# Performance work log

Hardware: AMD Instinct MI355X
Metric: run time of the kernel (lower is better)

The kernel has to match this reference:

```python
import jax, jax.numpy as jnp
import numpy as np

TOP_K = 2  # cfg.num_experts_per_tok
INIT_STD = 0.02


def setup_inputs() -> dict:
    key = jax.random.key(0)
    ks = jax.random.split(key, 6)
    B, S, D, F, E = 4, 2048, 1024, 4096, 8
    return {
        "residual": jax.random.normal(ks[0], (B, S, D), dtype=jnp.float32),
        "W_router": jax.random.normal(ks[1], (E, D), dtype=jnp.float32) * INIT_STD,
        "W_in": jax.random.normal(ks[2], (E, D, F), dtype=jnp.float32) * INIT_STD,
        "b_in": jnp.zeros((E, F), dtype=jnp.float32),
        "W_out": jax.random.normal(ks[3], (E, F, D), dtype=jnp.float32) * INIT_STD,
        "b_out": jnp.zeros((E, D), dtype=jnp.float32),
    }


def reference(residual, W_router, W_in, b_in, W_out, b_out):
    B, S, D = residual.shape
    E = W_router.shape[0]
    x = residual.reshape(-1, D)                      # [T, D], T = B*S

    # Router: softmax over experts, pick top-k, renormalize selected weights.
    logits = jnp.einsum('td,ed->te', x, W_router)    # [T, E]
    probs = jax.nn.softmax(logits, axis=-1)
    top_w, top_i = jax.lax.top_k(probs, TOP_K)       # [T, K]
    top_w = top_w / jnp.sum(top_w, axis=-1, keepdims=True)

    # Dense combine weights [T, E]; zero for non-selected experts.
    combine = jnp.sum(jax.nn.one_hot(top_i, E, dtype=x.dtype) * top_w[..., None], axis=1)

    # Weighted sum of expert MLP outputs (GELU experts, exact erf as in torch).
    y = jnp.zeros_like(x)
    for e in range(E):  # small fixed expert count
        h = jax.nn.gelu(x @ W_in[e] + b_in[e], approximate=False)   # [T, F]
        y = y + combine[:, e:e + 1] * (h @ W_out[e] + b_out[e])     # [T, D]
    return y.reshape(B, S, D)
```

## Files before the change

kernel.cpp:

```cpp
#include <hip/hip_runtime.h>
#include <hip/hip_bf16.h>
#include <math.h>

#define T_TOK 8192
#define DMODEL 1024
#define FFN 4096
#define NEXP 8
#define NSLOT (T_TOK * 2)
#define MAXT 136

typedef _Float16 f16;
typedef _Float16 half8 __attribute__((ext_vector_type(8)));
typedef _Float16 half4 __attribute__((ext_vector_type(4)));
typedef float f32x4 __attribute__((ext_vector_type(4)));
typedef unsigned int u32;

__device__ __forceinline__ void gll16(const void* g, void* l) {
  __builtin_amdgcn_global_load_lds(
      (const __attribute__((address_space(1))) u32*)g,
      (__attribute__((address_space(3))) u32*)l, 16, 0, 0);
}

__device__ __forceinline__ float gelu_fast(float v) {
  float x = fabsf(v) * 0.70710678118654752f;
  float t = 1.0f / (1.0f + 0.3275911f * x);
  float poly = ((((1.061405429f * t - 1.453152027f) * t + 1.421413741f) * t -
                 0.284496736f) * t + 0.254829592f) * t;
  float erf_ = 1.0f - poly * __expf(-x * x);
  erf_ = copysignf(erf_, v);
  return 0.5f * v * (1.0f + erf_);
}

__device__ __forceinline__ float gelu_exact(float v) {
  return 0.5f * v * (1.0f + erff(v * 0.70710678118654752f));
}

__device__ __forceinline__ bool decode_tile(const int* __restrict__ counts,
                                            int tm, int& e, int& row0,
                                            int& nrows) {
  int acc = 0, off = 0;
#pragma unroll
  for (int i = 0; i < NEXP; i++) {
    int c = counts[i];
    int nt = (c + 127) >> 7;
    if (tm < acc + nt) {
      int lt = tm - acc;
      e = i; row0 = off + lt * 128; nrows = min(128, c - lt * 128);
      return true;
    }
    acc += nt; off += c;
  }
  return false;
}

__device__ __forceinline__ void transq_tile(const float* __restrict__ ip,
                                            f16* __restrict__ op, int R, int C,
                                            int r0, int c0, char* smemraw) {
  float* tile = (float*)smemraw;
  int tid = threadIdx.x;
  int q = tid & 15;
  int rr = tid >> 4;
#pragma unroll
  for (int p = 0; p < 8; p++) {
    int row = rr + p * 16;
    f32x4 v = *(const f32x4*)(ip + (size_t)(r0 + row) * C + c0 + q * 4);
    int qs = (q + (row >> 3)) & 15;
    *(f32x4*)(tile + row * 64 + qs * 4) = v;
  }
  __syncthreads();
#pragma unroll
  for (int p = 0; p < 4; p++) {
    int idx = tid + p * 256;
    int c = idx >> 4;
    int b = idx & 15;
    half8 h;
#pragma unroll
    for (int i = 0; i < 8; i++) {
      int row = b * 8 + i;
      int qs = (((c >> 2) + b) & 15);
      h[i] = (f16)tile[row * 64 + qs * 4 + (c & 3)];
    }
    __builtin_nontemporal_store(h, (half8*)(op + (size_t)(c0 + c) * R + r0 + b * 8));
  }
}

__global__ __launch_bounds__(256) void prepA_k(
    const float* __restrict__ x, const float* __restrict__ Wr,
    const float* __restrict__ Wi,
    int* __restrict__ sel_e, float* __restrict__ sel_w,
    f16* __restrict__ xh, f16* __restrict__ WiT) {
  __shared__ __align__(16) char smem[32768];
  if (blockIdx.x < 4096) {
    int e = blockIdx.x >> 9;
    int idx = blockIdx.x & 511;
    int rt = idx >> 6, ct = idx & 63;
    transq_tile(Wi + (size_t)e * DMODEL * FFN, WiT + (size_t)e * DMODEL * FFN,
                DMODEL, FFN, rt * 128, ct * 64, smem);
  } else {
    int rb = blockIdx.x - 4096;
    int t = rb * 4 + (threadIdx.x >> 6);
    int lane = threadIdx.x & 63;
    const float* xp = x + (size_t)t * DMODEL;
    f16* xhp = xh + (size_t)t * DMODEL;
    float p[NEXP];
#pragma unroll
    for (int e = 0; e < NEXP; e++) p[e] = 0.f;
#pragma unroll
    for (int q = 0; q < 4; q++) {
      f32x4 xv = *(const f32x4*)(xp + q * 256 + lane * 4);
      half4 h;
      h[0] = (f16)xv[0]; h[1] = (f16)xv[1]; h[2] = (f16)xv[2]; h[3] = (f16)xv[3];
      *(half4*)(xhp + q * 256 + lane * 4) = h;
#pragma unroll
      for (int e = 0; e < NEXP; e++) {
        const f32x4 wv = *(const f32x4*)(Wr + e * DMODEL + q * 256 + lane * 4);
        p[e] += xv[0] * wv[0] + xv[1] * wv[1] + xv[2] * wv[2] + xv[3] * wv[3];
      }
    }
#pragma unroll
    for (int off = 32; off; off >>= 1) {
#pragma unroll
      for (int e = 0; e < NEXP; e++) p[e] += __shfl_xor(p[e], off);
    }
    if (lane == 0) {
      float l0 = -1e30f, l1 = -1e30f;
      int e0 = 0, e1 = 1;
#pragma unroll
      for (int e = 0; e < NEXP; e++) {
        if (p[e] > l0) { l1 = l0; e1 = e0; l0 = p[e]; e0 = e; }
        else if (p[e] > l1) { l1 = p[e]; e1 = e; }
      }
      float r = expf(l1 - l0);
      float inv = 1.f / (1.f + r);
      sel_e[t * 2] = e0;     sel_w[t * 2] = inv;
      sel_e[t * 2 + 1] = e1; sel_w[t * 2 + 1] = r * inv;
    }
  }
}

__global__ __launch_bounds__(256) void count64_k(const int* __restrict__ sel_e,
                                                 int* __restrict__ counts) {
  __shared__ int lc[NEXP];
  int tid = threadIdx.x;
  if (tid < NEXP) lc[tid] = 0;
  __syncthreads();
  int v = sel_e[blockIdx.x * 256 + tid];
  atomicAdd(&lc[v], 1);
  __syncthreads();
  if (tid < NEXP) atomicAdd(&counts[tid], lc[tid]);
}

__global__ __launch_bounds__(256) void scatter_k(
    const int* __restrict__ sel_e, const float* __restrict__ sel_w,
    const int* __restrict__ counts, int* fill,
    int* __restrict__ row_tok, float* __restrict__ row_w,
    int* __restrict__ inv) {
  int s = blockIdx.x * 256 + threadIdx.x;
  int e = sel_e[s];
  int offs = 0;
#pragma unroll
  for (int i = 0; i < NEXP; i++) offs += (i < e) ? counts[i] : 0;
  int pos = atomicAdd(&fill[e], 1);
  int r = offs + pos;
  row_tok[r] = s >> 1;
  row_w[r] = sel_w[s];
  inv[s] = r;
}

__global__ __launch_bounds__(256, 3) void gemm1_k(
    const f16* __restrict__ Xh, const f16* __restrict__ Wt,
    const float* __restrict__ b_in, f16* __restrict__ H,
    const int* __restrict__ meta,
    const float* __restrict__ Wo, f16* __restrict__ WoT) {
  __shared__ __align__(16) char smem[36864];

  if (blockIdx.x >= MAXT * 32) {
    int bid = blockIdx.x - MAXT * 32;
    int e = bid >> 9;
    int idx = bid & 511;
    int rt = idx >> 4, ct = idx & 15;
    transq_tile(Wo + (size_t)e * DMODEL * FFN, WoT + (size_t)e * DMODEL * FFN,
                FFN, DMODEL, rt * 128, ct * 64, smem);
    return;
  }
  int bid2 = blockIdx.x;
  int xcd = bid2 & 7, bidx = bid2 >> 3;
  int wg = xcd * ((MAXT * 32) >> 3) + bidx;
  int tm = wg >> 5;
  int n0 = (wg & 31) * 128;
  int e, row0, nrows;
  if (!decode_tile(meta, tm, e, row0, nrows)) return;
  const int* row_tok = meta + 1024 + 2 * NSLOT;

  int tid = threadIdx.x, lane = tid & 63, wid = tid >> 6;
  int wrow = wid >> 1, wcol = wid & 1;
  int l15 = lane & 15, l4 = lane >> 4;

  u32 aoffs[4], boffs[4];
#pragma unroll
  for (int p = 0; p < 4; p++) {
    int L = tid + p * 256;
    int row = L >> 3, ch = L & 7;
    int cs = ch ^ (row & 7);
    aoffs[p] = (u32)(row_tok[min(row0 + row, NSLOT - 1)] * (DMODEL * 2) + cs * 16);
    boffs[p] = (u32)((e * FFN + n0 + row) * (DMODEL * 2) + cs * 16);
  }
  const char* gA = (const char*)Xh;
  const char* gB = (const char*)Wt;

  f32x4 acc[4][4];
#pragma unroll
  for (int m = 0; m < 4; m++)
#pragma unroll
    for (int n = 0; n < 4; n++) acc[m][n] = (f32x4)0.f;

  const int NT = DMODEL / 64;
  for (int kt = 0; kt < NT; ++kt) {
#pragma unroll
    for (int p = 0; p < 4; p++) {
      gll16(gA + aoffs[p], smem + (tid + p * 256) * 16);
      gll16(gB + boffs[p], smem + 16384 + (tid + p * 256) * 16);
      aoffs[p] += 128; boffs[p] += 128;
    }
    __syncthreads();
#pragma unroll
    for (int s = 0; s < 2; s++) {
      int swz = ((s * 4 + l4) ^ (l15 & 7)) << 4;
      const char* pA = smem + (wrow * 64 + l15) * 128 + swz;
      const char* pB = smem + 16384 + (wcol * 64 + l15) * 128 + swz;
      half8 a[4], b[4];
#pragma unroll
      for (int i = 0; i < 4; i++) a[i] = *(const half8*)(pA + i * 2048);
#pragma unroll
      for (int j = 0; j < 4; j++) b[j] = *(const half8*)(pB + j * 2048);
#pragma unroll
      for (int i = 0; i < 4; i++)
#pragma unroll
        for (int j = 0; j < 4; j++)
          acc[i][j] = __builtin_amdgcn_mfma_f32_16x16x32_f16(a[i], b[j], acc[i][j], 0, 0, 0);
    }
    __syncthreads();
  }

  char* wsm = smem + wid * 9216;
  float bias[4];
#pragma unroll
  for (int n = 0; n < 4; n++) bias[n] = b_in[e * FFN + n0 + wcol * 64 + n * 16 + l15];
#pragma unroll
  for (int m = 0; m < 4; m++)
#pragma unroll
    for (int n = 0; n < 4; n++)
#pragma unroll
      for (int j = 0; j < 4; j++) {
        int lrow = m * 16 + l4 * 4 + j;
        *(f16*)(wsm + lrow * 144 + (n * 16 + l15) * 2) =
            (f16)gelu_fast(acc[m][n][j] + bias[n]);
      }
#pragma unroll
  for (int p = 0; p < 8; ++p) {
    int lr = (lane >> 3) + p * 8;
    if (wrow * 64 + lr < nrows) {
      f32x4 v = *(const f32x4*)(wsm + lr * 144 + (lane & 7) * 16);
      __builtin_nontemporal_store(
          v, (f32x4*)(H + (size_t)(row0 + wrow * 64 + lr) * FFN + n0 +
                      wcol * 64 + (lane & 7) * 8));
    }
  }
}

__global__ __launch_bounds__(256, 3) void gemm2_k(
    const f16* __restrict__ H, const f16* __restrict__ Wt,
    const float* __restrict__ b_out, f16* __restrict__ Y0,
    f16* __restrict__ Y1, const int* __restrict__ meta) {
  int xcd = blockIdx.x & 7, bidx = blockIdx.x >> 3;
  int wg = xcd * (gridDim.x >> 3) + bidx;
  int tm = wg >> 4;
  int r4 = wg & 15;
  int n0 = (r4 & 7) * 128;
  int ks = r4 >> 3;
  int e, row0, nrows;
  if (!decode_tile(meta, tm, e, row0, nrows)) return;

  __shared__ __align__(16) char smem[36864];

  int tid = threadIdx.x, lane = tid & 63, wid = tid >> 6;
  int wrow = wid >> 1, wcol = wid & 1;
  int l15 = lane & 15, l4 = lane >> 4;
  u32 k0b = (u32)(ks * (FFN / 2) * 2);

  u32 aoffs[4], boffs[4];
#pragma unroll
  for (int p = 0; p < 4; p++) {
    int L = tid + p * 256;
    int row = L >> 3, ch = L & 7;
    int cs = ch ^ (row & 7);
    aoffs[p] = (u32)((u32)min(row0 + row, NSLOT - 1) * (FFN * 2) + k0b + cs * 16);
    boffs[p] = (u32)((u32)(e * DMODEL + n0 + row) * (FFN * 2) + k0b + cs * 16);
  }
  const char* gA = (const char*)H;
  const char* gB = (const char*)Wt;

  f32x4 acc[4][4];
#pragma unroll
  for (int m = 0; m < 4; m++)
#pragma unroll
    for (int n = 0; n < 4; n++) acc[m][n] = (f32x4)0.f;

  const int NT = (FFN / 2) / 64;
  for (int kt = 0; kt < NT; ++kt) {
#pragma unroll
    for (int p = 0; p < 4; p++) {
      gll16(gA + aoffs[p], smem + (tid + p * 256) * 16);
      gll16(gB + boffs[p], smem + 16384 + (tid + p * 256) * 16);
      aoffs[p] += 128; boffs[p] += 128;
    }
    __syncthreads();
#pragma unroll
    for (int s = 0; s < 2; s++) {
      int swz = ((s * 4 + l4) ^ (l15 & 7)) << 4;
      const char* pA = smem + (wrow * 64 + l15) * 128 + swz;
      const char* pB = smem + 16384 + (wcol * 64 + l15) * 128 + swz;
      half8 a[4], b[4];
#pragma unroll
      for (int i = 0; i < 4; i++) a[i] = *(const half8*)(pA + i * 2048);
#pragma unroll
      for (int j = 0; j < 4; j++) b[j] = *(const half8*)(pB + j * 2048);
#pragma unroll
      for (int i = 0; i < 4; i++)
#pragma unroll
        for (int j = 0; j < 4; j++)
          acc[i][j] = __builtin_amdgcn_mfma_f32_16x16x32_f16(a[i], b[j], acc[i][j], 0, 0, 0);
    }
    __syncthreads();
  }

  f16* Y = ks ? Y1 : Y0;
  char* wsm = smem + wid * 9216;
  float bias[4];
#pragma unroll
  for (int n = 0; n < 4; n++)
    bias[n] = (ks == 0) ? b_out[e * DMODEL + n0 + wcol * 64 + n * 16 + l15] : 0.f;
#pragma unroll
  for (int m = 0; m < 4; m++)
#pragma unroll
    for (int n = 0; n < 4; n++)
#pragma unroll
      for (int j = 0; j < 4; j++) {
        int lrow = m * 16 + l4 * 4 + j;
        *(f16*)(wsm + lrow * 144 + (n * 16 + l15) * 2) =
            (f16)(acc[m][n][j] + bias[n]);
      }
#pragma unroll
  for (int p = 0; p < 8; ++p) {
    int lr = (lane >> 3) + p * 8;
    if (wrow * 64 + lr < nrows) {
      f32x4 v = *(const f32x4*)(wsm + lr * 144 + (lane & 7) * 16);
      __builtin_nontemporal_store(
          v, (f32x4*)(Y + (size_t)(row0 + wrow * 64 + lr) * DMODEL + n0 +
                      wcol * 64 + (lane & 7) * 8));
    }
  }
}

__global__ __launch_bounds__(256) void combine_k(
    const f16* __restrict__ Y0, const f16* __restrict__ Y1,
    const int* __restrict__ inv, const float* __restrict__ row_w,
    float* __restrict__ out) {
  int t = blockIdx.x * 4 + (threadIdx.x >> 6);
  int lane = threadIdx.x & 63;
  int r0 = inv[2 * t], r1 = inv[2 * t + 1];
  float w0 = row_w[r0], w1 = row_w[r1];
  int d0 = lane * 16;
  const half8* a0 = (const half8*)(Y0 + (size_t)r0 * DMODEL + d0);
  const half8* a1 = (const half8*)(Y1 + (size_t)r0 * DMODEL + d0);
  const half8* b0 = (const half8*)(Y0 + (size_t)r1 * DMODEL + d0);
  const half8* b1 = (const half8*)(Y1 + (size_t)r1 * DMODEL + d0);
  float* op = out + (size_t)t * DMODEL + d0;
#pragma unroll
  for (int q = 0; q < 2; q++) {
    half8 x0 = a0[q], x1 = a1[q], y0 = b0[q], y1 = b1[q];
    float r[8];
#pragma unroll
    for (int i = 0; i < 8; i++)
      r[i] = w0 * ((float)x0[i] + (float)x1[i]) +
             w1 * ((float)y0[i] + (float)y1[i]);
    f32x4 v1 = {r[0], r[1], r[2], r[3]};
    f32x4 v2 = {r[4], r[5], r[6], r[7]};
    *(f32x4*)(op + q * 8) = v1;
    *(f32x4*)(op + q * 8 + 4) = v2;
  }
}

__global__ __launch_bounds__(256) void naive_k(
    const float* __restrict__ x, const float* __restrict__ W_in,
    const float* __restrict__ b_in, const float* __restrict__ W_out,
    const float* __restrict__ b_out, const int* __restrict__ sel_e,
    const float* __restrict__ sel_w, float* __restrict__ out) {
  int s = blockIdx.x;
  int t = s >> 1;
  int e = sel_e[s];
  float w = sel_w[s];
  __shared__ float xs[DMODEL];
  __shared__ float hs[FFN];
  int tid = threadIdx.x;
  for (int d = tid; d < DMODEL; d += 256) xs[d] = x[(size_t)t * DMODEL + d];
  __syncthreads();
  for (int f = tid; f < FFN; f += 256) {
    float a = b_in[e * FFN + f];
    const float* wp = W_in + (size_t)e * DMODEL * FFN + f;
    for (int d = 0; d < DMODEL; d++) a += xs[d] * wp[(size_t)d * FFN];
    hs[f] = gelu_exact(a);
  }
  __syncthreads();
  for (int d = tid; d < DMODEL; d += 256) {
    float a = b_out[e * DMODEL + d];
    const float* wp = W_out + (size_t)e * FFN * DMODEL + d;
    for (int f = 0; f < FFN; f++) a += hs[f] * wp[(size_t)f * DMODEL];
    atomicAdd(&out[(size_t)t * DMODEL + d], w * a);
  }
}

__global__ __launch_bounds__(256) void router_k(
    const float* __restrict__ x, const float* __restrict__ Wr,
    int* __restrict__ sel_e, float* __restrict__ sel_w) {
  int t = blockIdx.x * 4 + (threadIdx.x >> 6);
  int lane = threadIdx.x & 63;
  const float* xp = x + (size_t)t * DMODEL;
  float p[NEXP];
#pragma unroll
  for (int e = 0; e < NEXP; e++) p[e] = 0.f;
#pragma unroll
  for (int i = 0; i < DMODEL / 64; i++) {
    float xv = xp[lane + i * 64];
#pragma unroll
    for (int e = 0; e < NEXP; e++) p[e] += xv * Wr[e * DMODEL + lane + i * 64];
  }
#pragma unroll
  for (int off = 32; off; off >>= 1) {
#pragma unroll
    for (int e = 0; e < NEXP; e++) p[e] += __shfl_xor(p[e], off);
  }
  if (lane == 0) {
    float l0 = -1e30f, l1 = -1e30f;
    int e0 = 0, e1 = 1;
#pragma unroll
    for (int e = 0; e < NEXP; e++) {
      if (p[e] > l0) { l1 = l0; e1 = e0; l0 = p[e]; e0 = e; }
      else if (p[e] > l1) { l1 = p[e]; e1 = e; }
    }
    float r = expf(l1 - l0);
    float inv = 1.f / (1.f + r);
    sel_e[t * 2] = e0;     sel_w[t * 2] = inv;
    sel_e[t * 2 + 1] = e1; sel_w[t * 2 + 1] = r * inv;
  }
}

extern "C" void kernel_launch(void* const* d_in, const int* in_sizes, int n_in,
                              void* d_out, int out_size, void* d_ws, size_t ws_size,
                              hipStream_t stream) {
  const float* residual = (const float*)d_in[0];
  const float* W_router = (const float*)d_in[1];
  const float* W_in = (const float*)d_in[2];
  const float* b_in = (const float*)d_in[3];
  const float* W_out = (const float*)d_in[4];
  const float* b_out = (const float*)d_in[5];
  float* out = (float*)d_out;

  char* ws = (char*)d_ws;
  int* meta = (int*)ws;
  size_t off = (size_t)1 << 20;
  f16* Xh = (f16*)(ws + off); off += (size_t)T_TOK * DMODEL * 2;
  f16* Wih = (f16*)(ws + off); off += (size_t)NEXP * DMODEL * FFN * 2;
  f16* Woh = (f16*)(ws + off); off += (size_t)NEXP * DMODEL * FFN * 2;
  f16* H = (f16*)(ws + off); off += (size_t)NSLOT * FFN * 2;
  off += 65536;
  bool fast = ws_size >= off;

  f16* Y0 = Wih;
  f16* Y1 = Wih + (size_t)NSLOT * DMODEL;

  int* sel_e = meta + 1024;
  float* sel_w = (float*)(meta + 1024 + NSLOT);
  int* row_tok = meta + 1024 + 2 * NSLOT;
  float* row_w = (float*)(meta + 1024 + 3 * NSLOT);
  int* inv = meta + 1024 + 4 * NSLOT;

  if (fast) {
    hipMemsetAsync(meta, 0, 512, stream);
    prepA_k<<<4096 + T_TOK / 4, 256, 0, stream>>>(
        residual, W_router, W_in, sel_e, sel_w, Xh, Wih);
    count64_k<<<NSLOT / 256, 256, 0, stream>>>(sel_e, meta);
    scatter_k<<<NSLOT / 256, 256, 0, stream>>>(sel_e, sel_w, meta, meta + 64,
                                               row_tok, row_w, inv);
    gemm1_k<<<MAXT * 32 + 4096, 256, 0, stream>>>(Xh, Wih, b_in, H, meta,
                                                  W_out, Woh);
    gemm2_k<<<MAXT * 16, 256, 0, stream>>>(H, Woh, b_out, Y0, Y1, meta);
    combine_k<<<T_TOK / 4, 256, 0, stream>>>(Y0, Y1, inv, row_w, out);
  } else {
    hipMemsetAsync(d_out, 0, (size_t)out_size * sizeof(float), stream);
    router_k<<<T_TOK / 4, 256, 0, stream>>>(residual, W_router, sel_e, sel_w);
    naive_k<<<NSLOT, 256, 0, stream>>>(residual, W_in, b_in, W_out, b_out,
                                       sel_e, sel_w, out);
  }
}
```

Baseline: 512.6 us.

## Widen gemm1 tile to 128x256 with 512-thread blocks

Changes gemm1 from 256-thread blocks computing 128x128 tiles to 512-thread blocks (8 waves in a 2x4 grid) computing 128x256 tiles. Each A (token) tile is now reused across twice as many output columns, which halves the gathered A loads and the block count. The fused W_out transpose path gets a 512-thread variant, and the transposes now use plain stores instead of nontemporal ones. The 72KB shared memory request and launch_bounds(512,4) could limit occupancy or cause register spills.

```diff
diff --git a/kernel.cpp b/kernel.cpp
--- a/kernel.cpp
+++ b/kernel.cpp
@@ -53,16 +53,15 @@
   return false;
 }
 
-__device__ __forceinline__ void transq_tile(const float* __restrict__ ip,
-                                            f16* __restrict__ op, int R, int C,
-                                            int r0, int c0, char* smemraw) {
+__device__ __forceinline__ void transq_tile256(const float* __restrict__ ip,
+                                               f16* __restrict__ op, int R, int C,
+                                               int r0, int c0, char* smemraw) {
   float* tile = (float*)smemraw;
   int tid = threadIdx.x;
-  int q = tid & 15;
-  int rr = tid >> 4;
 #pragma unroll
   for (int p = 0; p < 8; p++) {
-    int row = rr + p * 16;
+    int idx = tid + p * 256;
+    int row = idx >> 4, q = idx & 15;
     f32x4 v = *(const f32x4*)(ip + (size_t)(r0 + row) * C + c0 + q * 4);
     int qs = (q + (row >> 3)) & 15;
     *(f32x4*)(tile + row * 64 + qs * 4) = v;
@@ -71,8 +70,7 @@
 #pragma unroll
   for (int p = 0; p < 4; p++) {
     int idx = tid + p * 256;
-    int c = idx >> 4;
-    int b = idx & 15;
+    int c = idx >> 4, b = idx & 15;
     half8 h;
 #pragma unroll
     for (int i = 0; i < 8; i++) {
@@ -80,7 +78,36 @@
       int qs = (((c >> 2) + b) & 15);
       h[i] = (f16)tile[row * 64 + qs * 4 + (c & 3)];
     }
-    __builtin_nontemporal_store(h, (half8*)(op + (size_t)(c0 + c) * R + r0 + b * 8));
+    *(half8*)(op + (size_t)(c0 + c) * R + r0 + b * 8) = h;
+  }
+}
+
+__device__ __forceinline__ void transq_tile512(const float* __restrict__ ip,
+                                               f16* __restrict__ op, int R, int C,
+                                               int r0, int c0, char* smemraw) {
+  float* tile = (float*)smemraw;
+  int tid = threadIdx.x;
+#pragma unroll
+  for (int p = 0; p < 4; p++) {
+    int idx = tid + p * 512;
+    int row = idx >> 4, q = idx & 15;
+    f32x4 v = *(const f32x4*)(ip + (size_t)(r0 + row) * C + c0 + q * 4);
+    int qs = (q + (row >> 3)) & 15;
+    *(f32x4*)(tile + row * 64 + qs * 4) = v;
+  }
+  __syncthreads();
+#pragma unroll
+  for (int p = 0; p < 2; p++) {
+    int idx = tid + p * 512;
+    int c = idx >> 4, b = idx & 15;
+    half8 h;
+#pragma unroll
+    for (int i = 0; i < 8; i++) {
+      int row = b * 8 + i;
+      int qs = (((c >> 2) + b) & 15);
+      h[i] = (f16)tile[row * 64 + qs * 4 + (c & 3)];
+    }
+    *(half8*)(op + (size_t)(c0 + c) * R + r0 + b * 8) = h;
   }
 }
 
@@ -94,8 +121,8 @@
     int e = blockIdx.x >> 9;
     int idx = blockIdx.x & 511;
     int rt = idx >> 6, ct = idx & 63;
-    transq_tile(Wi + (size_t)e * DMODEL * FFN, WiT + (size_t)e * DMODEL * FFN,
-                DMODEL, FFN, rt * 128, ct * 64, smem);
+    transq_tile256(Wi + (size_t)e * DMODEL * FFN, WiT + (size_t)e * DMODEL * FFN,
+                   DMODEL, FFN, rt * 128, ct * 64, smem);
   } else {
     int rb = blockIdx.x - 4096;
     int t = rb * 4 + (threadIdx.x >> 6);
@@ -167,42 +194,48 @@
   inv[s] = r;
 }
 
-__global__ __launch_bounds__(256, 3) void gemm1_k(
+__global__ __launch_bounds__(512, 4) void gemm1_k(
     const f16* __restrict__ Xh, const f16* __restrict__ Wt,
     const float* __restrict__ b_in, f16* __restrict__ H,
     const int* __restrict__ meta,
     const float* __restrict__ Wo, f16* __restrict__ WoT) {
-  __shared__ __align__(16) char smem[36864];
-
-  if (blockIdx.x >= MAXT * 32) {
-    int bid = blockIdx.x - MAXT * 32;
+  __shared__ __align__(16) char smem[73728];
+
+  if (blockIdx.x >= MAXT * 16) {
+    int bid = blockIdx.x - MAXT * 16;
     int e = bid >> 9;
     int idx = bid & 511;
     int rt = idx >> 4, ct = idx & 15;
-    transq_tile(Wo + (size_t)e * DMODEL * FFN, WoT + (size_t)e * DMODEL * FFN,
-                FFN, DMODEL, rt * 128, ct * 64, smem);
+    transq_tile512(Wo + (size_t)e * DMODEL * FFN, WoT + (size_t)e * DMODEL * FFN,
+                   FFN, DMODEL, rt * 128, ct * 64, smem);
     return;
   }
   int bid2 = blockIdx.x;
   int xcd = bid2 & 7, bidx = bid2 >> 3;
-  int wg = xcd * ((MAXT * 32) >> 3) + bidx;
-  int tm = wg >> 5;
-  int n0 = (wg & 31) * 128;
+  int wg = xcd * ((MAXT * 16) >> 3) + bidx;
+  int tm = wg >> 4;
+  int n0 = (wg & 15) * 256;
   int e, row0, nrows;
   if (!decode_tile(meta, tm, e, row0, nrows)) return;
   const int* row_tok = meta + 1024 + 2 * NSLOT;
 
   int tid = threadIdx.x, lane = tid & 63, wid = tid >> 6;
-  int wrow = wid >> 1, wcol = wid & 1;
+  int wrow = wid >> 2, wcol = wid & 3;
   int l15 = lane & 15, l4 = lane >> 4;
 
-  u32 aoffs[4], boffs[4];
-#pragma unroll
-  for (int p = 0; p < 4; p++) {
-    int L = tid + p * 256;
+  u32 aoffs[2], boffs[4];
+#pragma unroll
+  for (int p = 0; p < 2; p++) {
+    int L = tid + p * 512;
     int row = L >> 3, ch = L & 7;
     int cs = ch ^ (row & 7);
     aoffs[p] = (u32)(row_tok[min(row0 + row, NSLOT - 1)] * (DMODEL * 2) + cs * 16);
+  }
+#pragma unroll
+  for (int p = 0; p < 4; p++) {
+    int L = tid + p * 512;
+    int row = L >> 3, ch = L & 7;
+    int cs = ch ^ (row & 7);
     boffs[p] = (u32)((e * FFN + n0 + row) * (DMODEL * 2) + cs * 16);
   }
   const char* gA = (const char*)Xh;
@@ -217,10 +250,14 @@
   const int NT = DMODEL / 64;
   for (int kt = 0; kt < NT; ++kt) {
 #pragma unroll
+    for (int p = 0; p < 2; p++) {
+      gll16(gA + aoffs[p], smem + (tid + p * 512) * 16);
+      aoffs[p] += 128;
+    }
+#pragma unroll
     for (int p = 0; p < 4; p++) {
-      gll16(gA + aoffs[p], smem + (tid + p * 256) * 16);
-      gll16(gB + boffs[p], smem + 16384 + (tid + p * 256) * 16);
-      aoffs[p] += 128; boffs[p] += 128;
+      gll16(gB + boffs[p], smem + 16384 + (tid + p * 512) * 16);
+      boffs[p] += 128;
     }
     __syncthreads();
 #pragma unroll
@@ -492,7 +529,7 @@
     count64_k<<<NSLOT / 256, 256, 0, stream>>>(sel_e, meta);
     scatter_k<<<NSLOT / 256, 256, 0, stream>>>(sel_e, sel_w, meta, meta + 64,
                                                row_tok, row_w, inv);
-    gemm1_k<<<MAXT * 32 + 4096, 256, 0, stream>>>(Xh, Wih, b_in, H, meta,
+    gemm1_k<<<MAXT * 16 + 4096, 512, 0, stream>>>(Xh, Wih, b_in, H, meta,
                                                   W_out, Woh);
     gemm2_k<<<MAXT * 16, 256, 0, stream>>>(H, Woh, b_out, Y0, Y1, meta);
     combine_k<<<T_TOK / 4, 256, 0, stream>>>(Y0, Y1, inv, row_w, out);
```

Measured after the change: 515.9 us. No clear change (+0.7%).
